# Performance work log

Hardware: AMD Instinct MI355X
Metric: run time of the kernel (lower is better)

Reference implementation:

```python
import jax, jax.numpy as jnp
import numpy as np

EPS = 1e-8

def setup_inputs() -> dict:
    key = jax.random.key(0)
    k1, k2, k3, k4 = jax.random.split(key, 4)
    b, in_c, out_c, style_c, k, h, w = 8, 512, 512, 512, 3, 64, 64
    return {
        "input": jax.random.normal(k1, (b, in_c, h, w), dtype=jnp.float32),
        "style": jax.random.normal(k2, (b, style_c), dtype=jnp.float32),
        "w_affine": jax.random.normal(k3, (in_c, style_c), dtype=jnp.float32),  # Linear weight, init N(0,1), runtime-scaled
        "b_affine": jnp.ones((1, in_c), dtype=jnp.float32),                     # Bias init_value=1.0
        "w_conv": jax.random.normal(k4, (out_c, in_c, k, k), dtype=jnp.float32),
    }

def reference(input, style, w_affine, b_affine, w_conv):
    b, in_c, h, w = input.shape
    out_c, _, kh, kw = w_conv.shape
    # Equalized-LR runtime scales (lr_mul=1):
    affine_scale = 1.0 / (w_affine.shape[1] ** 0.5)          # he_std for Linear
    conv_scale = 1.0 / ((in_c * kh * kw) ** 0.5)             # he_std for conv weight
    # affine: Linear + Bias (bias initialized to 1.0)
    s = style @ w_affine.T * affine_scale + b_affine          # [b, in_c]
    # modulate: per-sample weight tensor [b, out_c, in_c, kh, kw]
    wgt = s[:, None, :, None, None] * (w_conv * conv_scale)[None]
    # demodulate
    demod = jax.lax.rsqrt(jnp.sum(wgt * wgt, axis=(2, 3, 4), keepdims=True) + EPS)
    wgt = wgt * demod
    # grouped conv with groups = batch (stride=1, padding=1)
    x = input.reshape(1, b * in_c, h, w)
    wgt = wgt.reshape(b * out_c, in_c, kh, kw)
    out = jax.lax.conv_general_dilated(
        x, wgt,
        window_strides=(1, 1),
        padding=[(1, 1), (1, 1)],
        dimension_numbers=("NCHW", "OIHW", "NCHW"),
        feature_group_count=b,
    )
    return out.reshape(b, out_c, h, w)
```

## Files before the change

kernel.cpp:

```cpp
#include <hip/hip_runtime.h>
#include <hip/hip_bf16.h>

#define BB 8
#define CIN 512
#define COUT 512
#define HH 64
#define WW 64

#define AFF_SCALE 0.044194173824159216f
#define CONV_SCALE 0.014731391274719736f
#define CONV_SCALE2 (1.0f/4608.0f)

typedef short s16x8 __attribute__((ext_vector_type(8)));
typedef float f32x4 __attribute__((ext_vector_type(4)));

__device__ __forceinline__ unsigned short f2bf(float f) {
  __hip_bfloat16 h = __float2bfloat16(f);
  return *reinterpret_cast<unsigned short*>(&h);
}

__device__ __forceinline__ void gload_lds16(const void* g, void* l) {
  __builtin_amdgcn_global_load_lds(
      (const __attribute__((address_space(1))) unsigned int*)g,
      (__attribute__((address_space(3))) unsigned int*)l, 16, 0, 0);
}

__global__ __launch_bounds__(256) void affine_kernel(
    const float* __restrict__ style, const float* __restrict__ wa,
    const float* __restrict__ ba, float* __restrict__ smod) {
  int wid  = (blockIdx.x << 2) + (threadIdx.x >> 6);
  int lane = threadIdx.x & 63;
  int b  = wid >> 9;
  int ic = wid & 511;
  const float* s = style + b * CIN;
  const float* w = wa + (size_t)ic * CIN;
  float sum = 0.f;
#pragma unroll
  for (int k = 0; k < CIN / 64; ++k) sum += s[lane + 64 * k] * w[lane + 64 * k];
#pragma unroll
  for (int off = 32; off; off >>= 1) sum += __shfl_down(sum, off, 64);
  if (lane == 0) smod[wid] = sum * AFF_SCALE + ba[ic];
}

__global__ __launch_bounds__(256) void wsq_kernel(
    const float* __restrict__ wc, float* __restrict__ wsq) {
  int i = blockIdx.x * 256 + threadIdx.x;
  const float* p = wc + (size_t)i * 9;
  float s = 0.f;
#pragma unroll
  for (int k = 0; k < 9; ++k) { float v = p[k]; s += v * v; }
  wsq[i] = s;
}

__global__ __launch_bounds__(256) void demod_kernel(
    const float* __restrict__ smod, const float* __restrict__ wsq,
    float* __restrict__ demod) {
  int wid  = (blockIdx.x << 2) + (threadIdx.x >> 6);
  int lane = threadIdx.x & 63;
  int b  = wid >> 9;
  int oc = wid & 511;
  const float* s = smod + b * CIN;
  const float* w = wsq + (size_t)oc * CIN;
  float sum = 0.f;
#pragma unroll
  for (int k = 0; k < CIN / 64; ++k) {
    float sv = s[lane + 64 * k];
    sum += sv * sv * w[lane + 64 * k];
  }
#pragma unroll
  for (int off = 32; off; off >>= 1) sum += __shfl_down(sum, off, 64);
  if (lane == 0) demod[wid] = rsqrtf(sum * CONV_SCALE2 + 1e-8f) * CONV_SCALE;
}

__global__ __launch_bounds__(256) void premod_kernel(
    const float* __restrict__ xin, const float* __restrict__ smod,
    ushort* __restrict__ xt) {
  int n = blockIdx.x * 256 + threadIdx.x;
  int kg = n & 3;
  int x  = (n >> 2) & 63;
  int y  = (n >> 8) & 63;
  int g  = (n >> 14) & 15;
  int b  = n >> 18;
  int ic0 = g * 32 + kg * 8;
  const float* sp = smod + b * CIN + ic0;
  const float* xp = xin + (((size_t)b * CIN + ic0) * HH + y) * WW + x;
  s16x8 o;
#pragma unroll
  for (int j = 0; j < 8; ++j) {
    float v = xp[(size_t)j * HH * WW] * sp[j];
    o[j] = (short)f2bf(v);
  }
  *(s16x8*)(xt + (size_t)n * 8) = o;
}

__global__ __launch_bounds__(256) void wpack_kernel(
    const float* __restrict__ wc, ushort* __restrict__ wfrag) {
  int n = blockIdx.x * 256 + threadIdx.x;
  int l = n & 63;
  int rem = n >> 6;
  int ocg = rem & 31;
  int rem2 = rem >> 5;
  int tap = rem2 % 9;
  int g   = rem2 / 9;
  int oc  = ocg * 16 + (l & 15);
  int ic0 = g * 32 + (l >> 4) * 8;
  int kh = tap / 3, kw = tap - kh * 3;
  s16x8 o;
#pragma unroll
  for (int j = 0; j < 8; ++j) {
    float v = wc[((size_t)oc * CIN + ic0 + j) * 9 + kh * 3 + kw];
    o[j] = (short)f2bf(v);
  }
  *(s16x8*)(wfrag + (size_t)n * 8) = o;
}

#define XS_ROW 4224
#define XS_BUF (6 * XS_ROW)

__global__ __launch_bounds__(256, 2) void conv_mfma(
    const ushort* __restrict__ xt,
    const ushort* __restrict__ wfrag,
    const float* __restrict__ demod,
    float* __restrict__ out) {
  __shared__ char lds[2 * XS_BUF];

  int tid = threadIdx.x;
  int l = tid & 63, w = tid >> 6;
  int bid = blockIdx.x;
  int ocb = bid & 3;
  int b   = (bid >> 2) & 7;
  int yt  = bid >> 5;
  int y0  = yt * 4;

  f32x4 acc[8][4];
#pragma unroll
  for (int i = 0; i < 8; ++i)
#pragma unroll
    for (int j = 0; j < 4; ++j) acc[i][j] = f32x4{0.f, 0.f, 0.f, 0.f};

  if (tid < 96) {
    int buf = tid & 1, side = (tid >> 1) & 1, kgz = (tid >> 2) & 3, r = tid >> 4;
    int chunk = side ? (260 + kgz) : kgz;
    *(int4*)(lds + buf * XS_BUF + r * XS_ROW + chunk * 16) = int4{0, 0, 0, 0};
  }
  if (y0 == 0) {
    for (int i = tid; i < 512; i += 256) {
      int buf = i & 1, chunk = 4 + (i >> 1);
      *(int4*)(lds + buf * XS_BUF + chunk * 16) = int4{0, 0, 0, 0};
    }
  }
  if (y0 == 60) {
    for (int i = tid; i < 512; i += 256) {
      int buf = i & 1, chunk = 4 + (i >> 1);
      *(int4*)(lds + buf * XS_BUF + 5 * XS_ROW + chunk * 16) = int4{0, 0, 0, 0};
    }
  }

  int lm = l & 15, kg = l >> 4;
  int boffs[4][3];
#pragma unroll
  for (int fn = 0; fn < 4; ++fn)
#pragma unroll
    for (int dxi = 0; dxi < 3; ++dxi) {
      int col = fn * 16 + lm + dxi;
      boffs[fn][dxi] = (col * 4 + (kg ^ ((col >> 1) & 3))) * 16;
    }

  int col_s = 1 + w * 16 + (l >> 2);
  int srcoff = (col_s - 1) * 64 + ((l & 3) ^ ((col_s >> 1) & 3)) * 16;
  int lds_woff = 64 + w * 1024;

  const char* xtb = (const char*)xt;
  const char* wl = (const char*)wfrag + (size_t)(ocb * 8) * 1024 + (size_t)l * 16;

  s16x8 wH[3][4];
#pragma unroll
  for (int q = 0; q < 4; ++q) wH[0][q] = *(const s16x8*)(wl + q * 1024);
#pragma unroll
  for (int q = 0; q < 4; ++q) wH[1][q] = *(const s16x8*)(wl + 4096 + q * 1024);

  {
    size_t gbase = (size_t)(b * 16) * 262144;
#pragma unroll
    for (int r = 0; r < 6; ++r) {
      int gy = y0 - 1 + r;
      if (gy >= 0 && gy < HH)
        gload_lds16(xtb + gbase + (size_t)gy * 4096 + srcoff,
                    lds + r * XS_ROW + lds_woff);
    }
  }
  __syncthreads();

  for (int g2 = 0; g2 < 8; ++g2) {
    const char* wg = wl + (size_t)g2 * 589824;
#pragma unroll
    for (int gg = 0; gg < 2; ++gg) {
      char* xs_r = lds + gg * XS_BUF;
      char* xs_w = lds + (gg ^ 1) * XS_BUF;
#pragma unroll
      for (int tap = 0; tap < 9; ++tap) {
        const int X0 = 2 * (gg * 9 + tap);

        if (tap == 6 && (gg == 0 || g2 < 7)) {
          __builtin_amdgcn_sched_barrier(0);
          size_t gbase = (size_t)(b * 16 + g2 * 2 + gg + 1) * 262144;
#pragma unroll
          for (int r = 0; r < 6; ++r) {
            int gy = y0 - 1 + r;
            if (gy >= 0 && gy < HH)
              gload_lds16(xtb + gbase + (size_t)gy * 4096 + srcoff,
                          xs_w + r * XS_ROW + lds_woff);
          }
          __builtin_amdgcn_sched_barrier(0);
        }

        const int dy = tap / 3 - 1, dxi = tap % 3;
        const int rb = w + 1 + dy;
        s16x8 bfr[4];
#pragma unroll
        for (int fn = 0; fn < 4; ++fn)
          bfr[fn] = *(const s16x8*)(xs_r + rb * XS_ROW + boffs[fn][dxi]);

        {
          const int u = X0 % 3, v = (X0 + 2) % 3;
          const char* wp = wg + (size_t)((X0 + 2) >> 1) * 32768 + ((X0 + 2) & 1) * 4096;
#pragma unroll
          for (int q = 0; q < 4; ++q) wH[v][q] = *(const s16x8*)(wp + q * 1024);
          __builtin_amdgcn_s_setprio(1);
#pragma unroll
          for (int q = 0; q < 4; ++q)
#pragma unroll
            for (int fn = 0; fn < 4; ++fn)
              acc[q][fn] = __builtin_amdgcn_mfma_f32_16x16x32_bf16(wH[u][q], bfr[fn], acc[q][fn], 0, 0, 0);
          __builtin_amdgcn_s_setprio(0);
        }
        {
          const int u = (X0 + 1) % 3, v = (X0 + 3) % 3;
          const char* wp = wg + (size_t)((X0 + 3) >> 1) * 32768 + ((X0 + 3) & 1) * 4096;
#pragma unroll
          for (int q = 0; q < 4; ++q) wH[v][q] = *(const s16x8*)(wp + q * 1024);
          __builtin_amdgcn_s_setprio(1);
#pragma unroll
          for (int q = 0; q < 4; ++q)
#pragma unroll
            for (int fn = 0; fn < 4; ++fn)
              acc[4 + q][fn] = __builtin_amdgcn_mfma_f32_16x16x32_bf16(wH[u][q], bfr[fn], acc[4 + q][fn], 0, 0, 0);
          __builtin_amdgcn_s_setprio(0);
        }

        if (tap == 8 && (gg == 0 || g2 < 7)) {
          __builtin_amdgcn_sched_barrier(0);
          asm volatile("s_waitcnt vmcnt(0) lgkmcnt(0)" ::: "memory");
          __builtin_amdgcn_sched_barrier(0);
          __builtin_amdgcn_s_barrier();
          __builtin_amdgcn_sched_barrier(0);
        }
      }
    }
  }

  int oc_base = ocb * 128;
  int gy = y0 + w;
#pragma unroll
  for (int fm = 0; fm < 8; ++fm) {
#pragma unroll
    for (int r = 0; r < 4; ++r) {
      int oc = oc_base + fm * 16 + (l >> 4) * 4 + r;
      float dm = demod[b * COUT + oc];
#pragma unroll
      for (int fn = 0; fn < 4; ++fn) {
        out[(((size_t)b * COUT + oc) * 4096) + gy * 64 + fn * 16 + (l & 15)] =
            acc[fm][fn][r] * dm;
      }
    }
  }
}

extern "C" void kernel_launch(void* const* d_in, const int* in_sizes, int n_in,
                              void* d_out, int out_size, void* d_ws, size_t ws_size,
                              hipStream_t stream) {
  const float* input = (const float*)d_in[0];
  const float* style = (const float*)d_in[1];
  const float* wa    = (const float*)d_in[2];
  const float* ba    = (const float*)d_in[3];
  const float* wconv = (const float*)d_in[4];
  float* out = (float*)d_out;

  float* smod  = (float*)d_ws;
  float* demod = smod + BB * CIN;
  float* wsq   = demod + BB * COUT;
  ushort* wfrag = (ushort*)(wsq + (size_t)COUT * CIN);
  ushort* xt    = wfrag + (size_t)16 * 9 * 32 * 64 * 8;

  affine_kernel<<<BB * CIN / 4, 256, 0, stream>>>(style, wa, ba, smod);
  wsq_kernel<<<COUT * CIN / 256, 256, 0, stream>>>(wconv, wsq);
  demod_kernel<<<BB * COUT / 4, 256, 0, stream>>>(smod, wsq, demod);
  wpack_kernel<<<16 * 9 * 32 * 64 / 256, 256, 0, stream>>>(wconv, wfrag);
  premod_kernel<<<BB * 16 * 64 * 64 * 4 / 256, 256, 0, stream>>>(input, smod, xt);
  conv_mfma<<<BB * 4 * 16, 256, 0, stream>>>(xt, wfrag, demod, out);
}
```

Baseline: 160.8 us.

## Switch conv MFMA from 16x16x32 to 32x32x16 bf16 tiles with repacked weights

Replaces the 16x16x32 bf16 MFMA tiling with 32x32x16 instructions. The weight fragment packing, LDS B-operand offsets, accumulator layout and output store mapping are all reworked to match the new instruction shape. Fewer, larger MFMAs need fewer B-fragment LDS reads per FLOP. The end-of-stage wait is also relaxed from vmcnt(0) lgkmcnt(0) to vmcnt(8), so in-flight weight prefetches are no longer drained at each barrier; this risks a correctness hazard if the LDS staging loads are not guaranteed complete.

```diff
diff --git a/kernel.cpp b/kernel.cpp
--- a/kernel.cpp
+++ b/kernel.cpp
@@ -13,6 +13,7 @@
 
 typedef short s16x8 __attribute__((ext_vector_type(8)));
 typedef float f32x4 __attribute__((ext_vector_type(4)));
+typedef float f32x16 __attribute__((ext_vector_type(16)));
 
 __device__ __forceinline__ unsigned short f2bf(float f) {
   __hip_bfloat16 h = __float2bfloat16(f);
@@ -96,15 +97,14 @@
 __global__ __launch_bounds__(256) void wpack_kernel(
     const float* __restrict__ wc, ushort* __restrict__ wfrag) {
   int n = blockIdx.x * 256 + threadIdx.x;
-  int l = n & 63;
-  int rem = n >> 6;
-  int ocg = rem & 31;
-  int rem2 = rem >> 5;
-  int tap = rem2 % 9;
-  int g   = rem2 / 9;
-  int oc  = ocg * 16 + (l & 15);
-  int ic0 = g * 32 + (l >> 4) * 8;
+  int l    = n & 63;
+  int ks   = (n >> 6) & 1;
+  int mf   = (n >> 7) & 15;
+  int widx = n >> 11;
+  int g = widx / 9, tap = widx % 9;
   int kh = tap / 3, kw = tap - kh * 3;
+  int oc  = mf * 32 + (l & 31);
+  int ic0 = g * 32 + ks * 16 + 8 * (l >> 5);
   s16x8 o;
 #pragma unroll
   for (int j = 0; j < 8; ++j) {
@@ -132,11 +132,13 @@
   int yt  = bid >> 5;
   int y0  = yt * 4;
 
-  f32x4 acc[8][4];
-#pragma unroll
-  for (int i = 0; i < 8; ++i)
-#pragma unroll
-    for (int j = 0; j < 4; ++j) acc[i][j] = f32x4{0.f, 0.f, 0.f, 0.f};
+  f32x16 acc[4][2];
+#pragma unroll
+  for (int i = 0; i < 4; ++i)
+#pragma unroll
+    for (int j = 0; j < 2; ++j)
+#pragma unroll
+      for (int e = 0; e < 16; ++e) acc[i][j][e] = 0.f;
 
   if (tid < 96) {
     int buf = tid & 1, side = (tid >> 1) & 1, kgz = (tid >> 2) & 3, r = tid >> 4;
@@ -156,28 +158,33 @@
     }
   }
 
-  int lm = l & 15, kg = l >> 4;
-  int boffs[4][3];
-#pragma unroll
-  for (int fn = 0; fn < 4; ++fn)
-#pragma unroll
-    for (int dxi = 0; dxi < 3; ++dxi) {
-      int col = fn * 16 + lm + dxi;
-      boffs[fn][dxi] = (col * 4 + (kg ^ ((col >> 1) & 3))) * 16;
-    }
+  int boffs[2][3][2];
+  {
+    int lm = l & 31, kh2 = l >> 5;
+#pragma unroll
+    for (int fn = 0; fn < 2; ++fn)
+#pragma unroll
+      for (int dxi = 0; dxi < 3; ++dxi)
+#pragma unroll
+        for (int ks = 0; ks < 2; ++ks) {
+          int col = fn * 32 + lm + dxi;
+          int kg  = kh2 + 2 * ks;
+          boffs[fn][dxi][ks] = (col * 4 + (kg ^ ((col >> 1) & 3))) * 16;
+        }
+  }
 
   int col_s = 1 + w * 16 + (l >> 2);
   int srcoff = (col_s - 1) * 64 + ((l & 3) ^ ((col_s >> 1) & 3)) * 16;
   int lds_woff = 64 + w * 1024;
 
   const char* xtb = (const char*)xt;
-  const char* wl = (const char*)wfrag + (size_t)(ocb * 8) * 1024 + (size_t)l * 16;
+  const char* wl = (const char*)wfrag + (size_t)ocb * 8192 + (size_t)l * 16;
 
   s16x8 wH[3][4];
 #pragma unroll
-  for (int q = 0; q < 4; ++q) wH[0][q] = *(const s16x8*)(wl + q * 1024);
-#pragma unroll
-  for (int q = 0; q < 4; ++q) wH[1][q] = *(const s16x8*)(wl + 4096 + q * 1024);
+  for (int q = 0; q < 4; ++q) wH[0][q] = *(const s16x8*)(wl + q * 2048);
+#pragma unroll
+  for (int q = 0; q < 4; ++q) wH[1][q] = *(const s16x8*)(wl + q * 2048 + 1024);
 
   {
     size_t gbase = (size_t)(b * 16) * 262144;
@@ -216,41 +223,43 @@
 
         const int dy = tap / 3 - 1, dxi = tap % 3;
         const int rb = w + 1 + dy;
-        s16x8 bfr[4];
-#pragma unroll
-        for (int fn = 0; fn < 4; ++fn)
-          bfr[fn] = *(const s16x8*)(xs_r + rb * XS_ROW + boffs[fn][dxi]);
+        s16x8 bfr[2][2];
+#pragma unroll
+        for (int fn = 0; fn < 2; ++fn)
+#pragma unroll
+          for (int ks = 0; ks < 2; ++ks)
+            bfr[fn][ks] = *(const s16x8*)(xs_r + rb * XS_ROW + boffs[fn][dxi][ks]);
 
         {
           const int u = X0 % 3, v = (X0 + 2) % 3;
-          const char* wp = wg + (size_t)((X0 + 2) >> 1) * 32768 + ((X0 + 2) & 1) * 4096;
-#pragma unroll
-          for (int q = 0; q < 4; ++q) wH[v][q] = *(const s16x8*)(wp + q * 1024);
+          const char* wp = wg + (size_t)((X0 + 2) >> 1) * 32768 + ((X0 + 2) & 1) * 1024;
+#pragma unroll
+          for (int q = 0; q < 4; ++q) wH[v][q] = *(const s16x8*)(wp + q * 2048);
           __builtin_amdgcn_s_setprio(1);
 #pragma unroll
           for (int q = 0; q < 4; ++q)
 #pragma unroll
-            for (int fn = 0; fn < 4; ++fn)
-              acc[q][fn] = __builtin_amdgcn_mfma_f32_16x16x32_bf16(wH[u][q], bfr[fn], acc[q][fn], 0, 0, 0);
+            for (int fn = 0; fn < 2; ++fn)
+              acc[q][fn] = __builtin_amdgcn_mfma_f32_32x32x16_bf16(wH[u][q], bfr[fn][0], acc[q][fn], 0, 0, 0);
           __builtin_amdgcn_s_setprio(0);
         }
         {
           const int u = (X0 + 1) % 3, v = (X0 + 3) % 3;
-          const char* wp = wg + (size_t)((X0 + 3) >> 1) * 32768 + ((X0 + 3) & 1) * 4096;
-#pragma unroll
-          for (int q = 0; q < 4; ++q) wH[v][q] = *(const s16x8*)(wp + q * 1024);
+          const char* wp = wg + (size_t)((X0 + 3) >> 1) * 32768 + ((X0 + 3) & 1) * 1024;
+#pragma unroll
+          for (int q = 0; q < 4; ++q) wH[v][q] = *(const s16x8*)(wp + q * 2048);
           __builtin_amdgcn_s_setprio(1);
 #pragma unroll
           for (int q = 0; q < 4; ++q)
 #pragma unroll
-            for (int fn = 0; fn < 4; ++fn)
-              acc[4 + q][fn] = __builtin_amdgcn_mfma_f32_16x16x32_bf16(wH[u][q], bfr[fn], acc[4 + q][fn], 0, 0, 0);
+            for (int fn = 0; fn < 2; ++fn)
+              acc[q][fn] = __builtin_amdgcn_mfma_f32_32x32x16_bf16(wH[u][q], bfr[fn][1], acc[q][fn], 0, 0, 0);
           __builtin_amdgcn_s_setprio(0);
         }
 
         if (tap == 8 && (gg == 0 || g2 < 7)) {
           __builtin_amdgcn_sched_barrier(0);
-          asm volatile("s_waitcnt vmcnt(0) lgkmcnt(0)" ::: "memory");
+          asm volatile("s_waitcnt vmcnt(8)" ::: "memory");
           __builtin_amdgcn_sched_barrier(0);
           __builtin_amdgcn_s_barrier();
           __builtin_amdgcn_sched_barrier(0);
@@ -259,19 +268,19 @@
     }
   }
 
-  int oc_base = ocb * 128;
   int gy = y0 + w;
-#pragma unroll
-  for (int fm = 0; fm < 8; ++fm) {
-#pragma unroll
-    for (int r = 0; r < 4; ++r) {
-      int oc = oc_base + fm * 16 + (l >> 4) * 4 + r;
+  int colbase = l & 31;
+  int rowadd = 4 * (l >> 5);
+#pragma unroll
+  for (int q = 0; q < 4; ++q) {
+#pragma unroll
+    for (int reg = 0; reg < 16; ++reg) {
+      int row = (reg & 3) + 8 * (reg >> 2) + rowadd;
+      int oc = ocb * 128 + q * 32 + row;
       float dm = demod[b * COUT + oc];
-#pragma unroll
-      for (int fn = 0; fn < 4; ++fn) {
-        out[(((size_t)b * COUT + oc) * 4096) + gy * 64 + fn * 16 + (l & 15)] =
-            acc[fm][fn][r] * dm;
-      }
+      size_t obase = ((size_t)(b * COUT + oc)) * 4096 + gy * 64;
+      out[obase + colbase]      = acc[q][0][reg] * dm;
+      out[obase + 32 + colbase] = acc[q][1][reg] * dm;
     }
   }
 }
```

Result: no change. 162.2 us (+0.9%).
